# Performance work log

Hardware: AMD Instinct MI355X
Metric: run time of the kernel (lower is better)

The kernel has to match this reference:

```python
import jax, jax.numpy as jnp
from jax import lax
import numpy as np

BN_EPS = 1e-3  # ultralytics BatchNorm2d default eps

def setup_inputs() -> dict:
    key = jax.random.key(0)
    ks = jax.random.split(key, 6)
    B, C, H, W = 16, 64, 160, 160
    E, R = 4, 16  # experts, reduced router dim = C // reduction
    return {
        "x": jax.random.normal(ks[0], (B, C, H, W), jnp.float32),
        "fc1_w": jax.random.normal(ks[1], (R, C), jnp.float32) * 0.1,
        "fc2_w": jax.random.normal(ks[2], (E, R), jnp.float32) * 0.1,
        "fc2_b": jax.random.normal(ks[3], (E,), jnp.float32) * 0.1,
        "conv_w": jax.random.normal(ks[4], (E, C, C, 3, 3), jnp.float32) * 0.05,
        "bn_gamma": jnp.ones((E, C), jnp.float32),
        "bn_beta": jnp.zeros((E, C), jnp.float32),
        "bn_mean": jax.random.normal(ks[5], (E, C), jnp.float32) * 0.1,
        "bn_var": jnp.ones((E, C), jnp.float32),
    }

def reference(x, fc1_w, fc2_w, fc2_b, conv_w, bn_gamma, bn_beta, bn_mean, bn_var):
    # Router: global avg pool -> fc1 -> relu -> fc2 -> softmax over experts
    g = jnp.mean(x, axis=(2, 3))                       # [B, C]
    h = jax.nn.relu(g @ fc1_w.T)                       # [B, R]
    w = jax.nn.softmax(h @ fc2_w.T + fc2_b, axis=1)    # [B, E]

    def expert(kernel, gamma, beta, mean, var):
        # Conv2d(bias=False, pad=k//2) + BatchNorm2d (eval) + SiLU
        y = lax.conv_general_dilated(
            x, kernel, window_strides=(1, 1), padding="SAME",
            dimension_numbers=("NCHW", "OIHW", "NCHW"))
        scale = (gamma * lax.rsqrt(var + BN_EPS))[None, :, None, None]
        shift = (beta - mean * gamma * lax.rsqrt(var + BN_EPS))[None, :, None, None]
        return jax.nn.silu(y * scale + shift)          # [B, Co, H, W]

    outs = jax.vmap(expert)(conv_w, bn_gamma, bn_beta, bn_mean, bn_var)  # [E, B, Co, H, W]
    return jnp.einsum("ebchw,be->bchw", outs, w)
```

## Files before the change

kernel.cpp:

```cpp
#include <hip/hip_runtime.h>
#include <hip/hip_bf16.h>

typedef unsigned short u16;
typedef unsigned int   u32;
typedef __attribute__((ext_vector_type(8))) short s16x8;
typedef __attribute__((ext_vector_type(4))) float f32x4;

#define BN_EPS 1e-3f
#define NB 16
#define NC 64
#define NH 160
#define NW 160
#define NE 4
#define NR 16
#define HP 162
#define WPD 162

#define OFF_XT 0UL
#define SZ_XT  (16UL*162*162*64*2)
#define OFF_WT (OFF_XT + SZ_XT)
#define SZ_WT  (4UL*64*9*64*2)
#define OFF_SC (OFF_WT + SZ_WT)
#define OFF_SH (OFF_SC + 1024UL)
#define OFF_G  (OFF_SH + 1024UL)
#define OFF_WE (OFF_G + 4096UL)
#define OFF_GP (OFF_WE + 256UL)

#define XSTRIDE 342
#define XLS_BYTES (8 * XSTRIDE * 16)
#define WLS_BYTES (2304 * 16)
#define SMEM_TOTAL (XLS_BYTES + WLS_BYTES)

__device__ __forceinline__ u16 f2bf(float f) {
    u32 u = __builtin_bit_cast(u32, f);
    u += 0x7fffu + ((u >> 16) & 1u);
    return (u16)(u >> 16);
}

__global__ void prep_w(const float* __restrict__ cw, u16* __restrict__ wt,
                       const float* __restrict__ gamma, const float* __restrict__ beta,
                       const float* __restrict__ mean, const float* __restrict__ var,
                       float* __restrict__ scale, float* __restrict__ shift) {
    int idx = blockIdx.x * 256 + threadIdx.x;
    if (idx < 4 * 2 * 9 * 4 * 64 * 8) {
        int cin = idx & 7;
        int t = idx >> 3;
        int co = t & 63; t >>= 6;
        int cio = t & 3; t >>= 2;
        int tap = t % 9; t /= 9;
        int ch = t & 1;
        int e = t >> 1;
        int ci = ch * 32 + cio * 8 + cin;
        wt[idx] = f2bf(cw[(((long)(e * 64 + co)) * 64 + ci) * 9 + tap]);
    }
    if (idx < 256) {
        float sc = gamma[idx] * rsqrtf(var[idx] + BN_EPS);
        scale[idx] = sc;
        shift[idx] = beta[idx] - mean[idx] * sc;
    }
}

__global__ void prep_x(const float* __restrict__ x, u16* __restrict__ xt,
                       float* __restrict__ gpart) {
    __shared__ float tile[64][33];
    int blk = blockIdx.x;
    int t = threadIdx.x;
    if (blk >= 12800) {
        int bb = blk - 12800;
        int hp = bb % 162, b = bb / 162;
        u32* row = (u32*)xt + (((long)b * 162 + hp) * 162) * 32;
        if (hp == 0 || hp == 161) {
            for (int i = t; i < 162 * 32; i += 256) row[i] = 0u;
        } else if (t < 64) {
            int p = (t >> 5) ? 161 : 0;
            row[p * 32 + (t & 31)] = 0u;
        }
        return;
    }
    int wt5 = blk % 5;
    int tmp = blk / 5;
    int h = tmp % 160, b = tmp / 160;
    int w0 = wt5 * 32;
    int w = t & 31, c0 = t >> 5;
#pragma unroll
    for (int i = 0; i < 8; ++i) {
        int c = c0 + 8 * i;
        tile[c][w] = x[(((long)b * 64 + c) * 160 + h) * 160 + w0 + w];
    }
    __syncthreads();
    if (t < 64) {
        float s = 0.f;
#pragma unroll
        for (int wi = 0; wi < 32; ++wi) s += tile[t][wi];
        gpart[((long)(b * 64 + t)) * 800 + h * 5 + wt5] = s;
    }
    u32* xt32 = (u32*)xt;
    long base = ((((long)b * 162 + h + 1) * 162) + (w0 + 1)) * 32;
#pragma unroll
    for (int j = 0; j < 4; ++j) {
        int idx = t + 256 * j;
        int p = idx >> 5, cp = idx & 31;
        float v0 = tile[2 * cp][p], v1 = tile[2 * cp + 1][p];
        xt32[base + p * 32 + cp] = (u32)f2bf(v0) | ((u32)f2bf(v1) << 16);
    }
}

__global__ void g_reduce(const float* __restrict__ gpart, float* __restrict__ g) {
    int id = blockIdx.x;
    int t = threadIdx.x;
    float s = 0.f;
    for (int i = t; i < 800; i += 256) s += gpart[(long)id * 800 + i];
#pragma unroll
    for (int off = 32; off > 0; off >>= 1) s += __shfl_down(s, off, 64);
    __shared__ float red[4];
    if ((t & 63) == 0) red[t >> 6] = s;
    __syncthreads();
    if (t == 0) g[id] = (red[0] + red[1] + red[2] + red[3]) * (1.f / 25600.f);
}

__global__ void router(const float* __restrict__ g, const float* __restrict__ fc1w,
                       const float* __restrict__ fc2w, const float* __restrict__ fc2b,
                       float* __restrict__ wexp) {
    __shared__ float gL[16][64];
    __shared__ float h1[16][16];
    __shared__ float z[16][4];
    int t = threadIdx.x;
    for (int i = t; i < 1024; i += 256) gL[i >> 6][i & 63] = g[i];
    __syncthreads();
    {
        int b = t >> 4, r = t & 15;
        float s = 0.f;
#pragma unroll
        for (int c = 0; c < 64; ++c) s += gL[b][c] * fc1w[r * 64 + c];
        h1[b][r] = fmaxf(s, 0.f);
    }
    __syncthreads();
    if (t < 64) {
        int b = t >> 2, e = t & 3;
        float s = fc2b[e];
#pragma unroll
        for (int r = 0; r < 16; ++r) s += h1[b][r] * fc2w[e * 16 + r];
        z[b][e] = s;
    }
    __syncthreads();
    if (t < 16) {
        int b = t;
        float m = fmaxf(fmaxf(z[b][0], z[b][1]), fmaxf(z[b][2], z[b][3]));
        float e0 = __expf(z[b][0] - m), e1 = __expf(z[b][1] - m);
        float e2 = __expf(z[b][2] - m), e3 = __expf(z[b][3] - m);
        float inv = 1.f / (e0 + e1 + e2 + e3);
        wexp[b * 4 + 0] = e0 * inv; wexp[b * 4 + 1] = e1 * inv;
        wexp[b * 4 + 2] = e2 * inv; wexp[b * 4 + 3] = e3 * inv;
    }
}

__global__ __launch_bounds__(256, 2) void conv_main(
    const u16* __restrict__ xt, const u16* __restrict__ wt,
    const float* __restrict__ scale, const float* __restrict__ shift,
    const float* __restrict__ wexp, float* __restrict__ out) {
    extern __shared__ char smem[];
    u16* xls = (u16*)smem;
    u16* wls = (u16*)(smem + XLS_BYTES);

    const int o = blockIdx.x;
    const int blk = (o & 7) * 200 + (o >> 3);
    const int wt5 = blk % 5;
    const int tmp = blk / 5;
    const int ht = tmp % 20;
    const int b = tmp / 20;
    const int h0 = ht * 8, w0 = wt5 * 32;
    const int tid = threadIdx.x;
    const int lane = tid & 63;
    const int wv = tid >> 6;
    const int l15 = lane & 15, kl = lane >> 4;

    {
        const u16* xb = xt + (long)b * HP * WPD * 64;
        for (int c = tid; c < 2720; c += 256) {
            int P = c >> 3, cg = c & 7;
            int y = P / 34, px = P - y * 34;
            const u16* src = xb + (((long)(h0 + y) * WPD) + (w0 + px)) * 64 + cg * 8;
            s16x8 v = *(const s16x8*)src;
            *(s16x8*)(&xls[(cg * XSTRIDE + P) << 3]) = v;
        }
    }

    int Pbase[4];
#pragma unroll
    for (int nf = 0; nf < 4; ++nf)
        Pbase[nf] = (2 * wv + (nf >> 1)) * 34 + (nf & 1) * 16 + l15;

    const int oA = (kl * 64 + l15) << 3;

    f32x4 oacc[4][4];
#pragma unroll
    for (int i = 0; i < 4; ++i)
#pragma unroll
        for (int j = 0; j < 4; ++j) oacc[i][j] = (f32x4)(0.f);

#pragma unroll 1
    for (int e = 0; e < 4; ++e) {
        f32x4 acc[4][4];
#pragma unroll
        for (int i = 0; i < 4; ++i)
#pragma unroll
            for (int j = 0; j < 4; ++j) acc[i][j] = (f32x4)(0.f);

#pragma unroll 1
        for (int ch = 0; ch < 2; ++ch) {
            __syncthreads();
            {
                const u16* wsrc = wt + ((long)(e * 2 + ch)) * 2304 * 8;
#pragma unroll
                for (int r = 0; r < 9; ++r) {
                    int oo = r * 256 + tid;
                    __builtin_amdgcn_global_load_lds(
                        (const __attribute__((address_space(1))) void*)(wsrc + oo * 8),
                        (__attribute__((address_space(3))) void*)(wls + oo * 8),
                        16, 0, 0);
                }
            }
            int oB0 = (((ch * 4 + kl) * XSTRIDE) + Pbase[0]) << 3;
            int oB1 = (((ch * 4 + kl) * XSTRIDE) + Pbase[1]) << 3;
            int oB2 = (((ch * 4 + kl) * XSTRIDE) + Pbase[2]) << 3;
            int oB3 = (((ch * 4 + kl) * XSTRIDE) + Pbase[3]) << 3;

            auto tap_body = [&](int tap) {
                const int dy = tap / 3, dx = tap - 3 * dy;
                const int poff8 = (dy * 34 + dx) << 3;
                const int at = oA + tap * 2048;
                s16x8 af0 = *(const s16x8*)(&wls[at]);
                s16x8 af1 = *(const s16x8*)(&wls[at + 128]);
                s16x8 af2 = *(const s16x8*)(&wls[at + 256]);
                s16x8 af3 = *(const s16x8*)(&wls[at + 384]);
                s16x8 bf0 = *(const s16x8*)(&xls[oB0 + poff8]);
                s16x8 bf1 = *(const s16x8*)(&xls[oB1 + poff8]);
                s16x8 bf2 = *(const s16x8*)(&xls[oB2 + poff8]);
                s16x8 bf3 = *(const s16x8*)(&xls[oB3 + poff8]);
                acc[0][0] = __builtin_amdgcn_mfma_f32_16x16x32_bf16(af0, bf0, acc[0][0], 0, 0, 0);
                acc[1][0] = __builtin_amdgcn_mfma_f32_16x16x32_bf16(af1, bf0, acc[1][0], 0, 0, 0);
                acc[2][0] = __builtin_amdgcn_mfma_f32_16x16x32_bf16(af2, bf0, acc[2][0], 0, 0, 0);
                acc[3][0] = __builtin_amdgcn_mfma_f32_16x16x32_bf16(af3, bf0, acc[3][0], 0, 0, 0);
                acc[0][1] = __builtin_amdgcn_mfma_f32_16x16x32_bf16(af0, bf1, acc[0][1], 0, 0, 0);
                acc[1][1] = __builtin_amdgcn_mfma_f32_16x16x32_bf16(af1, bf1, acc[1][1], 0, 0, 0);
                acc[2][1] = __builtin_amdgcn_mfma_f32_16x16x32_bf16(af2, bf1, acc[2][1], 0, 0, 0);
                acc[3][1] = __builtin_amdgcn_mfma_f32_16x16x32_bf16(af3, bf1, acc[3][1], 0, 0, 0);
                acc[0][2] = __builtin_amdgcn_mfma_f32_16x16x32_bf16(af0, bf2, acc[0][2], 0, 0, 0);
                acc[1][2] = __builtin_amdgcn_mfma_f32_16x16x32_bf16(af1, bf2, acc[1][2], 0, 0, 0);
                acc[2][2] = __builtin_amdgcn_mfma_f32_16x16x32_bf16(af2, bf2, acc[2][2], 0, 0, 0);
                acc[3][2] = __builtin_amdgcn_mfma_f32_16x16x32_bf16(af3, bf2, acc[3][2], 0, 0, 0);
                acc[0][3] = __builtin_amdgcn_mfma_f32_16x16x32_bf16(af0, bf3, acc[0][3], 0, 0, 0);
                acc[1][3] = __builtin_amdgcn_mfma_f32_16x16x32_bf16(af1, bf3, acc[1][3], 0, 0, 0);
                acc[2][3] = __builtin_amdgcn_mfma_f32_16x16x32_bf16(af2, bf3, acc[2][3], 0, 0, 0);
                acc[3][3] = __builtin_amdgcn_mfma_f32_16x16x32_bf16(af3, bf3, acc[3][3], 0, 0, 0);
            };

            __builtin_amdgcn_s_waitcnt(0x074);
            __builtin_amdgcn_s_barrier();
            __builtin_amdgcn_sched_barrier(0);
#pragma unroll
            for (int tap = 0; tap < 5; ++tap) tap_body(tap);

            __builtin_amdgcn_s_waitcnt(0xF70);
            __builtin_amdgcn_s_barrier();
            __builtin_amdgcn_sched_barrier(0);
#pragma unroll
            for (int tap = 5; tap < 9; ++tap) tap_body(tap);
        }
        const float we = wexp[(b << 2) + e];
#pragma unroll
        for (int mf = 0; mf < 4; ++mf) {
#pragma unroll
            for (int j = 0; j < 4; ++j) {
                const int co = mf * 16 + (kl << 2) + j;
                const float sc = scale[(e << 6) + co];
                const float sh = shift[(e << 6) + co];
#pragma unroll
                for (int nf = 0; nf < 4; ++nf) {
                    float y = acc[mf][nf][j] * sc + sh;
                    float s = y * __builtin_amdgcn_rcpf(1.f + __expf(-y));
                    oacc[mf][nf][j] += we * s;
                }
            }
        }
    }
#pragma unroll
    for (int mf = 0; mf < 4; ++mf) {
#pragma unroll
        for (int nf = 0; nf < 4; ++nf) {
            const int y = h0 + 2 * wv + (nf >> 1);
            const int x = w0 + (nf & 1) * 16 + l15;
#pragma unroll
            for (int j = 0; j < 4; ++j) {
                const int co = mf * 16 + (kl << 2) + j;
                out[(((long)(b * 64 + co)) * 160 + y) * 160 + x] = oacc[mf][nf][j];
            }
        }
    }
}

extern "C" void kernel_launch(void* const* d_in, const int* in_sizes, int n_in,
                              void* d_out, int out_size, void* d_ws, size_t ws_size,
                              hipStream_t stream) {
    const float* x = (const float*)d_in[0];
    const float* fc1w = (const float*)d_in[1];
    const float* fc2w = (const float*)d_in[2];
    const float* fc2b = (const float*)d_in[3];
    const float* convw = (const float*)d_in[4];
    const float* gamma = (const float*)d_in[5];
    const float* beta = (const float*)d_in[6];
    const float* mean = (const float*)d_in[7];
    const float* var = (const float*)d_in[8];
    float* out = (float*)d_out;
    char* ws = (char*)d_ws;
    u16* xt = (u16*)(ws + OFF_XT);
    u16* wtb = (u16*)(ws + OFF_WT);
    float* scale = (float*)(ws + OFF_SC);
    float* shift = (float*)(ws + OFF_SH);
    float* g = (float*)(ws + OFF_G);
    float* wexp = (float*)(ws + OFF_WE);
    float* gpart = (float*)(ws + OFF_GP);

    hipFuncSetAttribute((const void*)conv_main,
                        hipFuncAttributeMaxDynamicSharedMemorySize, SMEM_TOTAL);

    prep_w<<<576, 256, 0, stream>>>(convw, wtb, gamma, beta, mean, var, scale, shift);
    prep_x<<<15392, 256, 0, stream>>>(x, xt, gpart);
    g_reduce<<<1024, 256, 0, stream>>>(gpart, g);
    router<<<1, 256, 0, stream>>>(g, fc1w, fc2w, fc2b, wexp);
    conv_main<<<1600, 256, SMEM_TOTAL, stream>>>(xt, wtb, scale, shift, wexp, out);
}
```

Baseline: 177.1 us.

## Switch conv to 32x32x16 MFMA, flatten expert loop, fuse prep and router kernels

The main conv kernel moves from 16x16x32 to 32x32x16 bf16 MFMA tiles with 16-wide accumulators. The expert/channel-half loops become one flat 8-stage loop, with the weight prefetch for stage 0 issued alongside the input tile load. Each expert's BN+SiLU epilogue is deferred to the start of the next expert's first stage. Separately, the weight and input prep kernels merge into one launch, and the g-reduce plus router become a single 16-block kernel, cutting launches. Larger MFMA tiles cut LDS reads per FLOP but raise accumulator register pressure under launch bounds of 2 blocks per SM.

```diff
diff --git a/kernel.cpp b/kernel.cpp
--- a/kernel.cpp
+++ b/kernel.cpp
@@ -4,15 +4,13 @@
 typedef unsigned short u16;
 typedef unsigned int   u32;
 typedef __attribute__((ext_vector_type(8))) short s16x8;
-typedef __attribute__((ext_vector_type(4))) float f32x4;
+typedef __attribute__((ext_vector_type(16))) float f32x16;
 
 #define BN_EPS 1e-3f
 #define NB 16
 #define NC 64
 #define NH 160
 #define NW 160
-#define NE 4
-#define NR 16
 #define HP 162
 #define WPD 162
 
@@ -22,8 +20,7 @@
 #define SZ_WT  (4UL*64*9*64*2)
 #define OFF_SC (OFF_WT + SZ_WT)
 #define OFF_SH (OFF_SC + 1024UL)
-#define OFF_G  (OFF_SH + 1024UL)
-#define OFF_WE (OFF_G + 4096UL)
+#define OFF_WE (OFF_SH + 1024UL)
 #define OFF_GP (OFF_WE + 256UL)
 
 #define XSTRIDE 342
@@ -37,34 +34,35 @@
     return (u16)(u >> 16);
 }
 
-__global__ void prep_w(const float* __restrict__ cw, u16* __restrict__ wt,
-                       const float* __restrict__ gamma, const float* __restrict__ beta,
-                       const float* __restrict__ mean, const float* __restrict__ var,
-                       float* __restrict__ scale, float* __restrict__ shift) {
-    int idx = blockIdx.x * 256 + threadIdx.x;
-    if (idx < 4 * 2 * 9 * 4 * 64 * 8) {
-        int cin = idx & 7;
-        int t = idx >> 3;
-        int co = t & 63; t >>= 6;
-        int cio = t & 3; t >>= 2;
-        int tap = t % 9; t /= 9;
-        int ch = t & 1;
-        int e = t >> 1;
-        int ci = ch * 32 + cio * 8 + cin;
-        wt[idx] = f2bf(cw[(((long)(e * 64 + co)) * 64 + ci) * 9 + tap]);
-    }
-    if (idx < 256) {
-        float sc = gamma[idx] * rsqrtf(var[idx] + BN_EPS);
-        scale[idx] = sc;
-        shift[idx] = beta[idx] - mean[idx] * sc;
-    }
-}
-
-__global__ void prep_x(const float* __restrict__ x, u16* __restrict__ xt,
-                       float* __restrict__ gpart) {
+__global__ void prep_all(const float* __restrict__ x, u16* __restrict__ xt,
+                         float* __restrict__ gpart,
+                         const float* __restrict__ cw, u16* __restrict__ wt,
+                         const float* __restrict__ gamma, const float* __restrict__ beta,
+                         const float* __restrict__ mean, const float* __restrict__ var,
+                         float* __restrict__ scale, float* __restrict__ shift) {
     __shared__ float tile[64][33];
     int blk = blockIdx.x;
     int t = threadIdx.x;
+    if (blk >= 15392) {
+        int idx = (blk - 15392) * 256 + t;
+        {
+            int cin = idx & 7;
+            int r = idx >> 3;
+            int co = r & 63; r >>= 6;
+            int cio = r & 3; r >>= 2;
+            int tap = r % 9; r /= 9;
+            int ch = r & 1;
+            int e = r >> 1;
+            int ci = ch * 32 + cio * 8 + cin;
+            wt[idx] = f2bf(cw[(((long)(e * 64 + co)) * 64 + ci) * 9 + tap]);
+        }
+        if (idx < 256) {
+            float sc = gamma[idx] * rsqrtf(var[idx] + BN_EPS);
+            scale[idx] = sc;
+            shift[idx] = beta[idx] - mean[idx] * sc;
+        }
+        return;
+    }
     if (blk >= 12800) {
         int bb = blk - 12800;
         int hp = bb % 162, b = bb / 162;
@@ -105,49 +103,42 @@
     }
 }
 
-__global__ void g_reduce(const float* __restrict__ gpart, float* __restrict__ g) {
-    int id = blockIdx.x;
-    int t = threadIdx.x;
+__global__ void router16(const float* __restrict__ gpart,
+                         const float* __restrict__ fc1w, const float* __restrict__ fc2w,
+                         const float* __restrict__ fc2b, float* __restrict__ wexp) {
+    __shared__ float part[256];
+    __shared__ float gl[64];
+    __shared__ float h1[16];
+    int b = blockIdx.x, t = threadIdx.x;
+    int c = t >> 2, q = t & 3;
+    const float* gp = gpart + ((long)(b * 64 + c)) * 800;
     float s = 0.f;
-    for (int i = t; i < 800; i += 256) s += gpart[(long)id * 800 + i];
-#pragma unroll
-    for (int off = 32; off > 0; off >>= 1) s += __shfl_down(s, off, 64);
-    __shared__ float red[4];
-    if ((t & 63) == 0) red[t >> 6] = s;
+    for (int i = q; i < 800; i += 4) s += gp[i];
+    part[t] = s;
     __syncthreads();
-    if (t == 0) g[id] = (red[0] + red[1] + red[2] + red[3]) * (1.f / 25600.f);
-}
-
-__global__ void router(const float* __restrict__ g, const float* __restrict__ fc1w,
-                       const float* __restrict__ fc2w, const float* __restrict__ fc2b,
-                       float* __restrict__ wexp) {
-    __shared__ float gL[16][64];
-    __shared__ float h1[16][16];
-    __shared__ float z[16][4];
-    int t = threadIdx.x;
-    for (int i = t; i < 1024; i += 256) gL[i >> 6][i & 63] = g[i];
-    __syncthreads();
-    {
-        int b = t >> 4, r = t & 15;
-        float s = 0.f;
-#pragma unroll
-        for (int c = 0; c < 64; ++c) s += gL[b][c] * fc1w[r * 64 + c];
-        h1[b][r] = fmaxf(s, 0.f);
-    }
-    __syncthreads();
-    if (t < 64) {
-        int b = t >> 2, e = t & 3;
-        float s = fc2b[e];
-#pragma unroll
-        for (int r = 0; r < 16; ++r) s += h1[b][r] * fc2w[e * 16 + r];
-        z[b][e] = s;
-    }
+    if (t < 64)
+        gl[t] = (part[4 * t] + part[4 * t + 1] + part[4 * t + 2] + part[4 * t + 3])
+                * (1.f / 25600.f);
     __syncthreads();
     if (t < 16) {
-        int b = t;
-        float m = fmaxf(fmaxf(z[b][0], z[b][1]), fmaxf(z[b][2], z[b][3]));
-        float e0 = __expf(z[b][0] - m), e1 = __expf(z[b][1] - m);
-        float e2 = __expf(z[b][2] - m), e3 = __expf(z[b][3] - m);
+        float v = 0.f;
+#pragma unroll
+        for (int c2 = 0; c2 < 64; ++c2) v += gl[c2] * fc1w[t * 64 + c2];
+        h1[t] = fmaxf(v, 0.f);
+    }
+    __syncthreads();
+    if (t == 0) {
+        float z[4];
+#pragma unroll
+        for (int e = 0; e < 4; ++e) {
+            float v = fc2b[e];
+#pragma unroll
+            for (int r = 0; r < 16; ++r) v += h1[r] * fc2w[e * 16 + r];
+            z[e] = v;
+        }
+        float m = fmaxf(fmaxf(z[0], z[1]), fmaxf(z[2], z[3]));
+        float e0 = __expf(z[0] - m), e1 = __expf(z[1] - m);
+        float e2 = __expf(z[2] - m), e3 = __expf(z[3] - m);
         float inv = 1.f / (e0 + e1 + e2 + e3);
         wexp[b * 4 + 0] = e0 * inv; wexp[b * 4 + 1] = e1 * inv;
         wexp[b * 4 + 2] = e2 * inv; wexp[b * 4 + 3] = e3 * inv;
@@ -172,8 +163,19 @@
     const int tid = threadIdx.x;
     const int lane = tid & 63;
     const int wv = tid >> 6;
-    const int l15 = lane & 15, kl = lane >> 4;
-
+    const int l31 = lane & 31, kh = lane >> 5;
+    const int r0 = 2 * wv;
+
+    {
+#pragma unroll
+        for (int r = 0; r < 9; ++r) {
+            int oo = r * 256 + tid;
+            __builtin_amdgcn_global_load_lds(
+                (const __attribute__((address_space(1))) void*)(wt + oo * 8),
+                (__attribute__((address_space(3))) void*)(wls + oo * 8),
+                16, 0, 0);
+        }
+    }
     {
         const u16* xb = xt + (long)b * HP * WPD * 64;
         for (int c = tid; c < 2720; c += 256) {
@@ -185,117 +187,105 @@
         }
     }
 
-    int Pbase[4];
-#pragma unroll
-    for (int nf = 0; nf < 4; ++nf)
-        Pbase[nf] = (2 * wv + (nf >> 1)) * 34 + (nf & 1) * 16 + l15;
-
-    const int oA = (kl * 64 + l15) << 3;
-
-    f32x4 oacc[4][4];
-#pragma unroll
-    for (int i = 0; i < 4; ++i)
-#pragma unroll
-        for (int j = 0; j < 4; ++j) oacc[i][j] = (f32x4)(0.f);
+    const int oA2 = (kh * 64 + l31) << 3;
+    const int oB_0 = ((kh * XSTRIDE) + (r0 + 0) * 34 + l31) << 3;
+    const int oB_1 = ((kh * XSTRIDE) + (r0 + 1) * 34 + l31) << 3;
+
+    f32x16 acc00 = (f32x16)(0.f), acc01 = (f32x16)(0.f);
+    f32x16 acc10 = (f32x16)(0.f), acc11 = (f32x16)(0.f);
+    f32x16 oac00 = (f32x16)(0.f), oac01 = (f32x16)(0.f);
+    f32x16 oac10 = (f32x16)(0.f), oac11 = (f32x16)(0.f);
+
+    auto epi = [&](int E) {
+        const float we = wexp[(b << 2) + E];
+        const float* scE = scale + (E << 6);
+        const float* shE = shift + (E << 6);
+#pragma unroll
+        for (int j = 0; j < 16; ++j) {
+            const int cob = (j & 3) + 8 * (j >> 2) + 4 * kh;
+            {
+                float sc = scE[cob], sh = shE[cob];
+                float y0 = acc00[j] * sc + sh;
+                float y1 = acc01[j] * sc + sh;
+                oac00[j] += we * (y0 * __builtin_amdgcn_rcpf(1.f + __expf(-y0)));
+                oac01[j] += we * (y1 * __builtin_amdgcn_rcpf(1.f + __expf(-y1)));
+            }
+            {
+                float sc = scE[cob + 32], sh = shE[cob + 32];
+                float y0 = acc10[j] * sc + sh;
+                float y1 = acc11[j] * sc + sh;
+                oac10[j] += we * (y0 * __builtin_amdgcn_rcpf(1.f + __expf(-y0)));
+                oac11[j] += we * (y1 * __builtin_amdgcn_rcpf(1.f + __expf(-y1)));
+            }
+        }
+        acc00 = (f32x16)(0.f); acc01 = (f32x16)(0.f);
+        acc10 = (f32x16)(0.f); acc11 = (f32x16)(0.f);
+    };
 
 #pragma unroll 1
-    for (int e = 0; e < 4; ++e) {
-        f32x4 acc[4][4];
-#pragma unroll
-        for (int i = 0; i < 4; ++i)
-#pragma unroll
-            for (int j = 0; j < 4; ++j) acc[i][j] = (f32x4)(0.f);
-
-#pragma unroll 1
-        for (int ch = 0; ch < 2; ++ch) {
+    for (int s = 0; s < 8; ++s) {
+        const int ch = s & 1;
+        if (s > 0) {
             __syncthreads();
-            {
-                const u16* wsrc = wt + ((long)(e * 2 + ch)) * 2304 * 8;
-#pragma unroll
-                for (int r = 0; r < 9; ++r) {
-                    int oo = r * 256 + tid;
-                    __builtin_amdgcn_global_load_lds(
-                        (const __attribute__((address_space(1))) void*)(wsrc + oo * 8),
-                        (__attribute__((address_space(3))) void*)(wls + oo * 8),
-                        16, 0, 0);
-                }
+            const u16* wsrc = wt + ((long)s) * 2304 * 8;
+#pragma unroll
+            for (int r = 0; r < 9; ++r) {
+                int oo = r * 256 + tid;
+                __builtin_amdgcn_global_load_lds(
+                    (const __attribute__((address_space(1))) void*)(wsrc + oo * 8),
+                    (__attribute__((address_space(3))) void*)(wls + oo * 8),
+                    16, 0, 0);
             }
-            int oB0 = (((ch * 4 + kl) * XSTRIDE) + Pbase[0]) << 3;
-            int oB1 = (((ch * 4 + kl) * XSTRIDE) + Pbase[1]) << 3;
-            int oB2 = (((ch * 4 + kl) * XSTRIDE) + Pbase[2]) << 3;
-            int oB3 = (((ch * 4 + kl) * XSTRIDE) + Pbase[3]) << 3;
-
-            auto tap_body = [&](int tap) {
-                const int dy = tap / 3, dx = tap - 3 * dy;
-                const int poff8 = (dy * 34 + dx) << 3;
-                const int at = oA + tap * 2048;
-                s16x8 af0 = *(const s16x8*)(&wls[at]);
-                s16x8 af1 = *(const s16x8*)(&wls[at + 128]);
-                s16x8 af2 = *(const s16x8*)(&wls[at + 256]);
-                s16x8 af3 = *(const s16x8*)(&wls[at + 384]);
-                s16x8 bf0 = *(const s16x8*)(&xls[oB0 + poff8]);
-                s16x8 bf1 = *(const s16x8*)(&xls[oB1 + poff8]);
-                s16x8 bf2 = *(const s16x8*)(&xls[oB2 + poff8]);
-                s16x8 bf3 = *(const s16x8*)(&xls[oB3 + poff8]);
-                acc[0][0] = __builtin_amdgcn_mfma_f32_16x16x32_bf16(af0, bf0, acc[0][0], 0, 0, 0);
-                acc[1][0] = __builtin_amdgcn_mfma_f32_16x16x32_bf16(af1, bf0, acc[1][0], 0, 0, 0);
-                acc[2][0] = __builtin_amdgcn_mfma_f32_16x16x32_bf16(af2, bf0, acc[2][0], 0, 0, 0);
-                acc[3][0] = __builtin_amdgcn_mfma_f32_16x16x32_bf16(af3, bf0, acc[3][0], 0, 0, 0);
-                acc[0][1] = __builtin_amdgcn_mfma_f32_16x16x32_bf16(af0, bf1, acc[0][1], 0, 0, 0);
-                acc[1][1] = __builtin_amdgcn_mfma_f32_16x16x32_bf16(af1, bf1, acc[1][1], 0, 0, 0);
-                acc[2][1] = __builtin_amdgcn_mfma_f32_16x16x32_bf16(af2, bf1, acc[2][1], 0, 0, 0);
-                acc[3][1] = __builtin_amdgcn_mfma_f32_16x16x32_bf16(af3, bf1, acc[3][1], 0, 0, 0);
-                acc[0][2] = __builtin_amdgcn_mfma_f32_16x16x32_bf16(af0, bf2, acc[0][2], 0, 0, 0);
-                acc[1][2] = __builtin_amdgcn_mfma_f32_16x16x32_bf16(af1, bf2, acc[1][2], 0, 0, 0);
-                acc[2][2] = __builtin_amdgcn_mfma_f32_16x16x32_bf16(af2, bf2, acc[2][2], 0, 0, 0);
-                acc[3][2] = __builtin_amdgcn_mfma_f32_16x16x32_bf16(af3, bf2, acc[3][2], 0, 0, 0);
-                acc[0][3] = __builtin_amdgcn_mfma_f32_16x16x32_bf16(af0, bf3, acc[0][3], 0, 0, 0);
-                acc[1][3] = __builtin_amdgcn_mfma_f32_16x16x32_bf16(af1, bf3, acc[1][3], 0, 0, 0);
-                acc[2][3] = __builtin_amdgcn_mfma_f32_16x16x32_bf16(af2, bf3, acc[2][3], 0, 0, 0);
-                acc[3][3] = __builtin_amdgcn_mfma_f32_16x16x32_bf16(af3, bf3, acc[3][3], 0, 0, 0);
-            };
-
-            __builtin_amdgcn_s_waitcnt(0x074);
-            __builtin_amdgcn_s_barrier();
-            __builtin_amdgcn_sched_barrier(0);
-#pragma unroll
-            for (int tap = 0; tap < 5; ++tap) tap_body(tap);
-
-            __builtin_amdgcn_s_waitcnt(0xF70);
-            __builtin_amdgcn_s_barrier();
-            __builtin_amdgcn_sched_barrier(0);
-#pragma unroll
-            for (int tap = 5; tap < 9; ++tap) tap_body(tap);
-        }
-        const float we = wexp[(b << 2) + e];
-#pragma unroll
-        for (int mf = 0; mf < 4; ++mf) {
-#pragma unroll
-            for (int j = 0; j < 4; ++j) {
-                const int co = mf * 16 + (kl << 2) + j;
-                const float sc = scale[(e << 6) + co];
-                const float sh = shift[(e << 6) + co];
-#pragma unroll
-                for (int nf = 0; nf < 4; ++nf) {
-                    float y = acc[mf][nf][j] * sc + sh;
-                    float s = y * __builtin_amdgcn_rcpf(1.f + __expf(-y));
-                    oacc[mf][nf][j] += we * s;
-                }
-            }
-        }
-    }
-#pragma unroll
-    for (int mf = 0; mf < 4; ++mf) {
-#pragma unroll
-        for (int nf = 0; nf < 4; ++nf) {
-            const int y = h0 + 2 * wv + (nf >> 1);
-            const int x = w0 + (nf & 1) * 16 + l15;
-#pragma unroll
-            for (int j = 0; j < 4; ++j) {
-                const int co = mf * 16 + (kl << 2) + j;
-                out[(((long)(b * 64 + co)) * 160 + y) * 160 + x] = oacc[mf][nf][j];
-            }
-        }
+        }
+        const int oBc0 = oB_0 + ((ch * 4 * XSTRIDE) << 3);
+        const int oBc1 = oB_1 + ((ch * 4 * XSTRIDE) << 3);
+
+        auto tap_body = [&](int tap) {
+            const int dy = tap / 3, dx = tap - 3 * dy;
+            const int pofU = (dy * 34 + dx) << 3;
+            const int atU = oA2 + tap * 2048;
+            s16x8 a00 = *(const s16x8*)(&wls[atU]);
+            s16x8 a10 = *(const s16x8*)(&wls[atU + 256]);
+            s16x8 a01 = *(const s16x8*)(&wls[atU + 1024]);
+            s16x8 a11 = *(const s16x8*)(&wls[atU + 1280]);
+            s16x8 b00 = *(const s16x8*)(&xls[oBc0 + pofU]);
+            s16x8 b10 = *(const s16x8*)(&xls[oBc1 + pofU]);
+            s16x8 b01 = *(const s16x8*)(&xls[oBc0 + pofU + 2 * XSTRIDE * 8]);
+            s16x8 b11 = *(const s16x8*)(&xls[oBc1 + pofU + 2 * XSTRIDE * 8]);
+            acc00 = __builtin_amdgcn_mfma_f32_32x32x16_bf16(a00, b00, acc00, 0, 0, 0);
+            acc10 = __builtin_amdgcn_mfma_f32_32x32x16_bf16(a10, b00, acc10, 0, 0, 0);
+            acc01 = __builtin_amdgcn_mfma_f32_32x32x16_bf16(a00, b10, acc01, 0, 0, 0);
+            acc11 = __builtin_amdgcn_mfma_f32_32x32x16_bf16(a10, b10, acc11, 0, 0, 0);
+            acc00 = __builtin_amdgcn_mfma_f32_32x32x16_bf16(a01, b01, acc00, 0, 0, 0);
+            acc10 = __builtin_amdgcn_mfma_f32_32x32x16_bf16(a11, b01, acc10, 0, 0, 0);
+            acc01 = __builtin_amdgcn_mfma_f32_32x32x16_bf16(a01, b11, acc01, 0, 0, 0);
+            acc11 = __builtin_amdgcn_mfma_f32_32x32x16_bf16(a11, b11, acc11, 0, 0, 0);
+        };
+
+        if (s == 0) __builtin_amdgcn_s_waitcnt(0x070);
+        else        __builtin_amdgcn_s_waitcnt(0x074);
+        __builtin_amdgcn_s_barrier();
+        __builtin_amdgcn_sched_barrier(0);
+        if (ch == 0 && s > 0) epi((s >> 1) - 1);
+#pragma unroll
+        for (int tap = 0; tap < 5; ++tap) tap_body(tap);
+
+        __builtin_amdgcn_s_waitcnt(0xF70);
+        __builtin_amdgcn_s_barrier();
+        __builtin_amdgcn_sched_barrier(0);
+#pragma unroll
+        for (int tap = 5; tap < 9; ++tap) tap_body(tap);
+    }
+    epi(3);
+
+    const int yy = h0 + r0;
+#pragma unroll
+    for (int j = 0; j < 16; ++j) {
+        const int cob = (j & 3) + 8 * (j >> 2) + 4 * kh;
+        out[(((long)(b * 64 + cob)) * 160 + yy) * 160 + w0 + l31] = oac00[j];
+        out[(((long)(b * 64 + cob)) * 160 + yy + 1) * 160 + w0 + l31] = oac01[j];
+        out[(((long)(b * 64 + cob + 32)) * 160 + yy) * 160 + w0 + l31] = oac10[j];
+        out[(((long)(b * 64 + cob + 32)) * 160 + yy + 1) * 160 + w0 + l31] = oac11[j];
     }
 }
 
@@ -317,16 +307,14 @@
     u16* wtb = (u16*)(ws + OFF_WT);
     float* scale = (float*)(ws + OFF_SC);
     float* shift = (float*)(ws + OFF_SH);
-    float* g = (float*)(ws + OFF_G);
     float* wexp = (float*)(ws + OFF_WE);
     float* gpart = (float*)(ws + OFF_GP);
 
     hipFuncSetAttribute((const void*)conv_main,
                         hipFuncAttributeMaxDynamicSharedMemorySize, SMEM_TOTAL);
 
-    prep_w<<<576, 256, 0, stream>>>(convw, wtb, gamma, beta, mean, var, scale, shift);
-    prep_x<<<15392, 256, 0, stream>>>(x, xt, gpart);
-    g_reduce<<<1024, 256, 0, stream>>>(gpart, g);
-    router<<<1, 256, 0, stream>>>(g, fc1w, fc2w, fc2b, wexp);
+    prep_all<<<15968, 256, 0, stream>>>(x, xt, gpart, convw, wtb,
+                                        gamma, beta, mean, var, scale, shift);
+    router16<<<16, 256, 0, stream>>>(gpart, fc1w, fc2w, fc2b, wexp);
     conv_main<<<1600, 256, SMEM_TOTAL, stream>>>(xt, wtb, scale, shift, wexp, out);
 }
```

New measurement: 194.1 us. +9.6%, slower.
